# Performance work log

Hardware: AMD Instinct MI355X
Metric: run time of the kernel (lower is better)

Reference implementation:

```python
import jax, jax.numpy as jnp
import numpy as np

# FlowNetC correlation params (fixed per init_kwargs)
PAD = 4
MAX_DISP = 4
STRIDE2 = 1
GRID_R = MAX_DISP // STRIDE2  # neighborhood grid radius -> 9x9 = 81 displacements


def setup_inputs() -> dict:
    key = jax.random.key(0)
    k1, k2 = jax.random.split(key)
    input1 = jax.random.normal(k1, (8, 256, 64, 128), dtype=jnp.float32)
    input2 = jax.random.normal(k2, (8, 256, 64, 128), dtype=jnp.float32)
    return {"input1": input1, "input2": input2}


def _correlation(input1, input2):
    B, C, H, W = input1.shape
    # pad input2 spatially by max_displacement (pad_size == max_displacement here)
    p2 = jnp.pad(input2, ((0, 0), (0, 0), (PAD, PAD), (PAD, PAD)))
    inv_nelems = jnp.asarray(1.0 / C, dtype=input1.dtype)  # K*K*C with K=1
    outs = []
    # fixed 9x9 displacement grid (structural loop, not a data-dim loop)
    for i in range(-GRID_R, GRID_R + 1):
        for j in range(-GRID_R, GRID_R + 1):
            dy = PAD + i * STRIDE2
            dx = PAD + j * STRIDE2
            shifted = jax.lax.dynamic_slice(p2, (0, 0, dy, dx), (B, C, H, W))
            # per-pixel dot product over channels
            outs.append(jnp.einsum('bchw,bchw->bhw', input1, shifted))
    out = jnp.stack(outs, axis=1) * inv_nelems  # [B, 81, H, W]
    return out


def reference(input1, input2):
    return _correlation(input1, input2)
```

## Files before the change

kernel.cpp:

```cpp
#include <hip/hip_runtime.h>


#define AS1 __attribute__((address_space(1)))
#define AS3 __attribute__((address_space(3)))

namespace {

constexpr int Cc = 256, Hh = 64, Ww = 128;
constexpr int HW = Hh * Ww;
constexpr int ND = 81;
constexpr int PBUF = 520;
constexpr int WREG = 2 * PBUF;

__device__ __forceinline__ void async16(const float* g, float* l) {
  __builtin_amdgcn_global_load_lds((const AS1 unsigned int*)g,
                                   (AS3 unsigned int*)l, 16, 0, 0);
}

__global__ __launch_bounds__(256, 3) void corr_kernel(
    const float* __restrict__ in1, const float* __restrict__ in2,
    float* __restrict__ out) {
  __shared__ __align__(16) float lds[4608];

  const int tid = threadIdx.x;
  const int w = tid >> 6;
  const int lane = tid & 63;
  const int q = lane & 15;
  const int cslo = lane >> 4;

  const int bid0 = blockIdx.x;
  const int nb = (bid0 & 7) * 576 + (bid0 >> 3);
  const int b = nb / 576;
  const int rem = nb - b * 576;
  const int h = rem / 9;
  const int dy = rem - h * 9;
  const int row2 = h + dy - 4;

  float* outbase = out + (((size_t)b * ND + (size_t)dy * 9) * Hh + h) * Ww;

  if ((unsigned)row2 >= (unsigned)Hh) {
    if (tid < 144) {
      const int dx = tid >> 4, qq = tid & 15;
      const float4 z = make_float4(0.f, 0.f, 0.f, 0.f);
      *(float4*)(outbase + (size_t)dx * HW + 8 * qq) = z;
      *(float4*)(outbase + (size_t)dx * HW + 8 * qq + 4) = z;
    }
    return;
  }

  const int wb = w * WREG;
  if (lane < 8) lds[wb + (lane >> 2) * PBUF + 512 + (lane & 3)] = 0.0f;

  int srcA, srcB;
  {
    const int s0 = lane, c0 = s0 >> 5, v0 = s0 & 31;
    const int vp0 = (v0 - 2 * c0) & 31;
    const int g0 = (vp0 < 16) ? (2 * vp0 + 1) : (2 * (vp0 - 16));
    srcA = (4 * w + c0) * HW + 4 * g0;
    const int s1 = 64 + lane, c1 = s1 >> 5, v1_ = s1 & 31;
    const int vp1 = (v1_ - 2 * c1) & 31;
    const int g1 = (vp1 < 16) ? (2 * vp1 + 1) : (2 * (vp1 - 16));
    srcB = (4 * w + c1) * HW + 4 * g1;
  }

  const int ro0 = (q == 0) ? 512 : (cslo * 32 + ((q - 1 + 2 * cslo) & 31)) * 4;
  const int ro1 = (cslo * 32 + ((16 + q + 2 * cslo) & 31)) * 4;
  const int ro2 = (cslo * 32 + ((q + 2 * cslo) & 31)) * 4;
  const int ro3 = (q == 15) ? 512 : (cslo * 32 + ((17 + q + 2 * cslo) & 31)) * 4;

  const float* in2row = in2 + ((size_t)b * Cc * Hh + row2) * Ww;
  const float* v1p =
      in1 + ((size_t)(b * Cc + 4 * w + cslo) * Hh + h) * Ww + 8 * q;

#define STAGE(P, BI)                                                   \
  {                                                                    \
    const float* s0_ = in2row + (size_t)(16 * (P)) * HW;               \
    async16(s0_ + srcA, &lds[wb + (BI) * PBUF]);                       \
    async16(s0_ + srcB, &lds[wb + (BI) * PBUF + 256]);                 \
  }

#define LOADV1(P, DST)                                                 \
  {                                                                    \
    const float* pp_ = v1p + (size_t)(16 * (P)) * HW;                  \
    const float4 a_ = *(const float4*)pp_;                             \
    const float4 d_ = *(const float4*)(pp_ + 4);                       \
    DST[0] = a_.x; DST[1] = a_.y; DST[2] = a_.z; DST[3] = a_.w;        \
    DST[4] = d_.x; DST[5] = d_.y; DST[6] = d_.z; DST[7] = d_.w;        \
  }

#define COMPUTE(BI, V1)                                                  \
  {                                                                      \
    const int bb_ = wb + (BI) * PBUF;                                    \
    const float4 A_ = *(const float4*)&lds[bb_ + ro0];       \
    const float4 B_ = *(const float4*)&lds[bb_ + ro1];       \
    const float4 C_ = *(const float4*)&lds[bb_ + ro2];       \
    const float4 D_ = *(const float4*)&lds[bb_ + ro3];       \
    const float t_[16] = {A_.x, A_.y, A_.z, A_.w, B_.x, B_.y, B_.z, B_.w,\
                          C_.x, C_.y, C_.z, C_.w, D_.x, D_.y, D_.z, D_.w};\
    _Pragma("unroll") for (int dx_ = 0; dx_ < 9; ++dx_)                  \
      _Pragma("unroll") for (int px_ = 0; px_ < 8; ++px_)                \
        acc[px_][dx_] = fmaf(V1[px_], t_[px_ + dx_], acc[px_][dx_]);     \
  }

#define VMCNT(N) asm volatile("s_waitcnt vmcnt(" #N ")" ::: "memory")

  float acc[8][9];
#pragma unroll
  for (int px = 0; px < 8; ++px)
#pragma unroll
    for (int dx = 0; dx < 9; ++dx) acc[px][dx] = 0.0f;

  float v1a[8], v1b[8];
  STAGE(0, 0); LOADV1(0, v1a);

#pragma unroll 1
  for (int pp = 0; pp < 16; pp += 2) {
    STAGE(pp + 1, 1); LOADV1(pp + 1, v1b);
    VMCNT(4);
    COMPUTE(0, v1a);
    if (pp + 2 < 16) {
      STAGE(pp + 2, 0); LOADV1(pp + 2, v1a);
      VMCNT(4);
    } else {
      VMCNT(0);
    }
    COMPUTE(1, v1b);
  }

#pragma unroll
  for (int px = 0; px < 8; ++px)
#pragma unroll
    for (int dx = 0; dx < 9; ++dx) {
      float v = acc[px][dx];
      v += __shfl_xor(v, 16, 64);
      v += __shfl_xor(v, 32, 64);
      acc[px][dx] = v;
    }

  __syncthreads();
  if (cslo == 0) {
    const int pb = (w * 16 + q) * 72;
#pragma unroll
    for (int dx = 0; dx < 9; ++dx) {
      *(float4*)&lds[pb + dx * 8] =
          make_float4(acc[0][dx], acc[1][dx], acc[2][dx], acc[3][dx]);
      *(float4*)&lds[pb + dx * 8 + 4] =
          make_float4(acc[4][dx], acc[5][dx], acc[6][dx], acc[7][dx]);
    }
  }
  __syncthreads();

  if (tid < 144) {
    const int dx = tid >> 4, qq = tid & 15;
    const float s = 1.0f / 256.0f;
    float r[8];
#pragma unroll
    for (int px = 0; px < 8; ++px) r[px] = 0.0f;
#pragma unroll
    for (int w4 = 0; w4 < 4; ++w4) {
      const int pb = ((w4 * 16 + qq) * 9 + dx) * 8;
      const float4 lo = *(const float4*)&lds[pb];
      const float4 hi = *(const float4*)&lds[pb + 4];
      r[0] += lo.x; r[1] += lo.y; r[2] += lo.z; r[3] += lo.w;
      r[4] += hi.x; r[5] += hi.y; r[6] += hi.z; r[7] += hi.w;
    }
    *(float4*)(outbase + (size_t)dx * HW + 8 * qq) =
        make_float4(r[0] * s, r[1] * s, r[2] * s, r[3] * s);
    *(float4*)(outbase + (size_t)dx * HW + 8 * qq + 4) =
        make_float4(r[4] * s, r[5] * s, r[6] * s, r[7] * s);
  }
}

}

extern "C" void kernel_launch(void* const* d_in, const int* in_sizes, int n_in,
                              void* d_out, int out_size, void* d_ws,
                              size_t ws_size, hipStream_t stream) {
  (void)in_sizes; (void)n_in; (void)out_size; (void)d_ws; (void)ws_size;
  const float* in1 = (const float*)d_in[0];
  const float* in2 = (const float*)d_in[1];
  float* outp = (float*)d_out;
  corr_kernel<<<4608, 256, 0, stream>>>(in1, in2, outp);
}
```

Before: 87.32 us.

## Deepen in2 async-LDS pipeline to four buffers and simplify LDS swizzle

Grows the per-wave LDS ring from two to four stages, so three channel-groups of input2 are in flight ahead of compute. The main loop is restructured into a prologue, a 4-way rotating steady state and an epilogue, with explicit vmcnt and lgkmcnt waits plus a sched barrier. It also replaces the interleaved, rotated LDS layout with a simpler contiguous rotation, which changes the bank-conflict pattern. The aim is to hide global-load latency. In exchange, LDS per block nearly doubles, which may limit occupancy against the 3-blocks-per-CU target.

```diff
diff --git a/kernel.cpp b/kernel.cpp
--- a/kernel.cpp
+++ b/kernel.cpp
@@ -10,7 +10,8 @@
 constexpr int HW = Hh * Ww;
 constexpr int ND = 81;
 constexpr int PBUF = 520;
-constexpr int WREG = 2 * PBUF;
+constexpr int NBUF = 4;
+constexpr int WREG = NBUF * PBUF;
 
 __device__ __forceinline__ void async16(const float* g, float* l) {
   __builtin_amdgcn_global_load_lds((const AS1 unsigned int*)g,
@@ -20,7 +21,7 @@
 __global__ __launch_bounds__(256, 3) void corr_kernel(
     const float* __restrict__ in1, const float* __restrict__ in2,
     float* __restrict__ out) {
-  __shared__ __align__(16) float lds[4608];
+  __shared__ __align__(16) float lds[8320];
 
   const int tid = threadIdx.x;
   const int w = tid >> 6;
@@ -49,24 +50,22 @@
   }
 
   const int wb = w * WREG;
-  if (lane < 8) lds[wb + (lane >> 2) * PBUF + 512 + (lane & 3)] = 0.0f;
+  if (lane < 16) lds[wb + (lane >> 2) * PBUF + 512 + (lane & 3)] = 0.0f;
 
   int srcA, srcB;
   {
-    const int s0 = lane, c0 = s0 >> 5, v0 = s0 & 31;
-    const int vp0 = (v0 - 2 * c0) & 31;
-    const int g0 = (vp0 < 16) ? (2 * vp0 + 1) : (2 * (vp0 - 16));
-    srcA = (4 * w + c0) * HW + 4 * g0;
-    const int s1 = 64 + lane, c1 = s1 >> 5, v1_ = s1 & 31;
-    const int vp1 = (v1_ - 2 * c1) & 31;
-    const int g1 = (vp1 < 16) ? (2 * vp1 + 1) : (2 * (vp1 - 16));
-    srcB = (4 * w + c1) * HW + 4 * g1;
+    const int c0 = lane >> 5;
+    srcA = (4 * w + c0) * HW + ((4 * (lane & 31) - 4 * c0) & 127);
+    const int c1 = 2 + (lane >> 5);
+    srcB = (4 * w + c1) * HW + ((4 * (lane & 31) - 4 * c1) & 127);
   }
 
-  const int ro0 = (q == 0) ? 512 : (cslo * 32 + ((q - 1 + 2 * cslo) & 31)) * 4;
-  const int ro1 = (cslo * 32 + ((16 + q + 2 * cslo) & 31)) * 4;
-  const int ro2 = (cslo * 32 + ((q + 2 * cslo) & 31)) * 4;
-  const int ro3 = (q == 15) ? 512 : (cslo * 32 + ((17 + q + 2 * cslo) & 31)) * 4;
+  const int ro0 =
+      (q == 0) ? 512 : (128 * cslo + ((8 * q - 4 + 4 * cslo) & 127));
+  const int ro1 = 128 * cslo + ((8 * q + 4 * cslo) & 127);
+  const int ro2 = 128 * cslo + ((8 * q + 4 + 4 * cslo) & 127);
+  const int ro3 =
+      (q == 15) ? 512 : (128 * cslo + ((8 * q + 8 + 4 * cslo) & 127));
 
   const float* in2row = in2 + ((size_t)b * Cc * Hh + row2) * Ww;
   const float* v1p =
@@ -74,9 +73,9 @@
 
 #define STAGE(P, BI)                                                   \
   {                                                                    \
-    const float* s0_ = in2row + (size_t)(16 * (P)) * HW;               \
-    async16(s0_ + srcA, &lds[wb + (BI) * PBUF]);                       \
-    async16(s0_ + srcB, &lds[wb + (BI) * PBUF + 256]);                 \
+    const float* s2_ = in2row + (size_t)(16 * (P)) * HW;               \
+    async16(s2_ + srcA, &lds[wb + (BI) * PBUF]);                       \
+    async16(s2_ + srcB, &lds[wb + (BI) * PBUF + 256]);                 \
   }
 
 #define LOADV1(P, DST)                                                 \
@@ -103,6 +102,9 @@
   }
 
 #define VMCNT(N) asm volatile("s_waitcnt vmcnt(" #N ")" ::: "memory")
+#define LGKM0                                             \
+  asm volatile("s_waitcnt lgkmcnt(0)" ::: "memory");      \
+  __builtin_amdgcn_sched_barrier(0)
 
   float acc[8][9];
 #pragma unroll
@@ -111,21 +113,22 @@
     for (int dx = 0; dx < 9; ++dx) acc[px][dx] = 0.0f;
 
   float v1a[8], v1b[8];
-  STAGE(0, 0); LOADV1(0, v1a);
+
+  LOADV1(0, v1a);
+  STAGE(0, 0); STAGE(1, 1); STAGE(2, 2);
+
+  LOADV1(1, v1b); STAGE(3, 3); VMCNT(8); COMPUTE(0, v1a); LGKM0;
 
 #pragma unroll 1
-  for (int pp = 0; pp < 16; pp += 2) {
-    STAGE(pp + 1, 1); LOADV1(pp + 1, v1b);
-    VMCNT(4);
-    COMPUTE(0, v1a);
-    if (pp + 2 < 16) {
-      STAGE(pp + 2, 0); LOADV1(pp + 2, v1a);
-      VMCNT(4);
-    } else {
-      VMCNT(0);
-    }
-    COMPUTE(1, v1b);
+  for (int pp = 1; pp <= 9; pp += 4) {
+    LOADV1(pp + 1, v1a); STAGE(pp + 3, 0); VMCNT(6); COMPUTE(1, v1b); LGKM0;
+    LOADV1(pp + 2, v1b); STAGE(pp + 4, 1); VMCNT(6); COMPUTE(2, v1a); LGKM0;
+    LOADV1(pp + 3, v1a); STAGE(pp + 5, 2); VMCNT(6); COMPUTE(3, v1b); LGKM0;
+    LOADV1(pp + 4, v1b); STAGE(pp + 6, 3); VMCNT(6); COMPUTE(0, v1a); LGKM0;
   }
+  LOADV1(14, v1a); VMCNT(4); COMPUTE(1, v1b); LGKM0;
+  LOADV1(15, v1b); VMCNT(2); COMPUTE(2, v1a); LGKM0;
+  VMCNT(0); COMPUTE(3, v1b);
 
 #pragma unroll
   for (int px = 0; px < 8; ++px)
```

Result: no change. 88.37 us (+1.2%).
